# Optimization experiments

Measured on AMD Instinct MI355X. Metric: run time of the kernel, lower is better.

Reference implementation:

```python
import jax, jax.numpy as jnp
import numpy as np


def setup_inputs() -> dict:
    key = jax.random.key(0)
    kq, kk, kv = jax.random.split(key, 3)
    B, S, D = 4, 4096, 128
    q = jax.random.normal(kq, (B, S, D), dtype=jnp.float32)
    k = jax.random.normal(kk, (B, S, D), dtype=jnp.float32)
    v = jax.random.normal(kv, (B, S, D), dtype=jnp.float32)
    return {"q_proj": q, "k_proj": k, "v_proj": v}


def reference(q_proj, k_proj, v_proj):
    # FlashAttention's online-softmax tiling computes exactly standard
    # softmax attention: softmax(Q K^T / sqrt(d)) V (no mask, non-causal).
    d = q_proj.shape[-1]
    scale = 1.0 / jnp.sqrt(jnp.asarray(d, dtype=q_proj.dtype))
    logits = jnp.einsum('bqd,bkd->bqk', q_proj, k_proj) * scale
    probs = jax.nn.softmax(logits, axis=-1)  # numerically stable (max-subtracted)
    out = jnp.einsum('bqk,bkd->bqd', probs, v_proj)
    return out
```

## Files before the change

kernel.cpp:

```cpp
#include <hip/hip_runtime.h>

#define BATCH 4
#define SEQ   4096
#define DIM   128
#define BM    64
#define BN    64
#define NGROUP 2
#define TPG (SEQ / (BN * NGROUP))

#define KS_STRIDE 128
#define VT_STRIDE 72

typedef __attribute__((ext_vector_type(8))) __bf16 bf16x8;
typedef __attribute__((ext_vector_type(8))) unsigned short u16x8;
typedef __attribute__((ext_vector_type(4))) unsigned int u32x4;
typedef __attribute__((ext_vector_type(4))) float f32x4;

__device__ __forceinline__ unsigned short f2bf(float f) {
    __bf16 h = (__bf16)f;
    return __builtin_bit_cast(unsigned short, h);
}

__device__ __forceinline__ bf16x8 lds_frag(const unsigned short* p) {
    u16x8 t = *(const u16x8*)p;
    return __builtin_bit_cast(bf16x8, t);
}

#define LDS_U16 (64 * KS_STRIDE + 128 * VT_STRIDE)

extern "C" __global__ __launch_bounds__(256, 2)
void fa_part(const float* __restrict__ q, const float* __restrict__ k,
             const float* __restrict__ v, float* __restrict__ out,
             float* __restrict__ lsum)
{
    __shared__ __align__(16) unsigned short lds[LDS_U16];
    unsigned short* Ks = lds;
    unsigned short* Vt = lds + 64 * KS_STRIDE;

    const int tid  = threadIdx.x;
    const int wq   = tid >> 6;
    const int lane = tid & 63;
    const int l16  = lane & 15;
    const int quad = lane >> 4;

    const int bid = blockIdx.x;
    const int c   = bid & 7;
    const int b   = c >> 1;
    const int g   = c & 1;
    const int q0  = (bid >> 3) * BM;

    const float scale = 0.08838834764831845f;

    const float4* q4 = (const float4*)q;
    const float4* k4 = (const float4*)k;

    bf16x8 qfrag[4];
#pragma unroll
    for (int kc = 0; kc < 4; ++kc) {
        const float4* qp = &q4[(b * SEQ + q0 + wq * 16 + l16) * 32 + kc * 8 + quad * 2];
        float4 f0 = qp[0], f1 = qp[1];
        u16x8 u;
        u[0] = f2bf(f0.x * scale); u[1] = f2bf(f0.y * scale);
        u[2] = f2bf(f0.z * scale); u[3] = f2bf(f0.w * scale);
        u[4] = f2bf(f1.x * scale); u[5] = f2bf(f1.y * scale);
        u[6] = f2bf(f1.z * scale); u[7] = f2bf(f1.w * scale);
        qfrag[kc] = __builtin_bit_cast(bf16x8, u);
    }

    const int kv0 = g * (SEQ / NGROUP);

    float4 ldK[8];
    float  ldV[4][8];
#pragma unroll
    for (int i = 0; i < 8; ++i) {
        int idx = tid + i * 256;
        ldK[i] = k4[(b * SEQ + kv0 + (idx >> 5)) * 32 + (idx & 31)];
    }
#pragma unroll
    for (int i = 0; i < 4; ++i) {
        int j = tid + i * 256, f = j & 127, kp8 = j >> 7;
        const float* vp = v + (size_t)(b * SEQ + kv0 + kp8 * 8) * DIM + f;
#pragma unroll
        for (int e = 0; e < 8; ++e) ldV[i][e] = vp[e * DIM];
    }

    float l_part = 0.f;
    f32x4 accO[8];
#pragma unroll
    for (int ob = 0; ob < 8; ++ob) accO[ob] = (f32x4){0.f, 0.f, 0.f, 0.f};

    for (int t = 0; t < TPG; ++t) {
        __syncthreads();

#pragma unroll
        for (int i = 0; i < 8; ++i) {
            int idx = tid + i * 256;
            int row = idx >> 5, c4 = idx & 31;
            float4 f = ldK[i];
            ushort4 u;
            u.x = f2bf(f.x); u.y = f2bf(f.y); u.z = f2bf(f.z); u.w = f2bf(f.w);
            *(ushort4*)&Ks[row * KS_STRIDE + ((c4 * 4) ^ (8 * (row & 7)))] = u;
        }
#pragma unroll
        for (int i = 0; i < 4; ++i) {
            int j = tid + i * 256, f = j & 127, kp8 = j >> 7;
            u16x8 u;
#pragma unroll
            for (int e = 0; e < 8; ++e) u[e] = f2bf(ldV[i][e]);
            *(u16x8*)&Vt[f * VT_STRIDE + kp8 * 8] = u;
        }
        __syncthreads();

        if (t + 1 < TPG) {
            const int kbase = kv0 + (t + 1) * BN;
#pragma unroll
            for (int i = 0; i < 8; ++i) {
                int idx = tid + i * 256;
                ldK[i] = k4[(b * SEQ + kbase + (idx >> 5)) * 32 + (idx & 31)];
            }
#pragma unroll
            for (int i = 0; i < 4; ++i) {
                int j = tid + i * 256, f = j & 127, kp8 = j >> 7;
                const float* vp = v + (size_t)(b * SEQ + kbase + kp8 * 8) * DIM + f;
#pragma unroll
                for (int e = 0; e < 8; ++e) ldV[i][e] = vp[e * DIM];
            }
        }

        f32x4 sacc[4];
#pragma unroll
        for (int nb = 0; nb < 4; ++nb) sacc[nb] = (f32x4){0.f, 0.f, 0.f, 0.f};
        __builtin_amdgcn_s_setprio(1);
#pragma unroll
        for (int kc = 0; kc < 4; ++kc) {
#pragma unroll
            for (int nb = 0; nb < 4; ++nb) {
                bf16x8 a = lds_frag(&Ks[(nb * 16 + l16) * KS_STRIDE +
                                        ((kc * 32 + quad * 8) ^ (8 * (l16 & 7)))]);
                sacc[nb] = __builtin_amdgcn_mfma_f32_16x16x32_bf16(a, qfrag[kc], sacc[nb], 0, 0, 0);
            }
        }
        __builtin_amdgcn_s_setprio(0);

        unsigned W[4][2];
#pragma unroll
        for (int nb = 0; nb < 4; ++nb)
#pragma unroll
            for (int s = 0; s < 2; ++s) {
                float e0 = __expf(sacc[nb][2 * s]);
                float e1 = __expf(sacc[nb][2 * s + 1]);
                l_part += e0 + e1;
                W[nb][s] = (unsigned)f2bf(e0) | ((unsigned)f2bf(e1) << 16);
            }

#pragma unroll
        for (int kk = 0; kk < 2; ++kk) {
            u32x4 wv;
#pragma unroll
            for (int w = 0; w < 4; ++w) {
                int src = l16 + 16 * (2 * (quad & 1) + (w >> 1));
                unsigned a0 = (unsigned)__shfl((int)W[kk * 2 + 0][w & 1], src);
                unsigned a1 = (unsigned)__shfl((int)W[kk * 2 + 1][w & 1], src);
                wv[w] = (quad & 2) ? a1 : a0;
            }
            bf16x8 pa = __builtin_bit_cast(bf16x8, wv);
            __builtin_amdgcn_s_setprio(1);
#pragma unroll
            for (int ob = 0; ob < 8; ++ob) {
                bf16x8 bb = lds_frag(&Vt[(ob * 16 + l16) * VT_STRIDE + kk * 32 + quad * 8]);
                accO[ob] = __builtin_amdgcn_mfma_f32_16x16x32_bf16(pa, bb, accO[ob], 0, 0, 0);
            }
            __builtin_amdgcn_s_setprio(0);
        }
    }

    {
        float s = l_part;
        s += __shfl_xor(s, 16);
        s += __shfl_xor(s, 32);
        if (quad == 0) atomicAdd(&lsum[b * SEQ + q0 + wq * 16 + l16], s);
    }
#pragma unroll
    for (int r = 0; r < 4; ++r) {
        const int row = b * SEQ + q0 + wq * 16 + quad * 4 + r;
        float* outp = out + (size_t)row * DIM;
#pragma unroll
        for (int ob = 0; ob < 8; ++ob)
            atomicAdd(&outp[ob * 16 + l16], accO[ob][r]);
    }
}

extern "C" __global__ void fa_norm(float* __restrict__ out, const float* __restrict__ lsum)
{
    int i = blockIdx.x * 256 + threadIdx.x;
    float inv = 1.0f / lsum[i >> 5];
    float4* o4 = (float4*)out;
    float4 vv = o4[i];
    vv.x *= inv; vv.y *= inv; vv.z *= inv; vv.w *= inv;
    o4[i] = vv;
}

extern "C" void kernel_launch(void* const* d_in, const int* in_sizes, int n_in,
                              void* d_out, int out_size, void* d_ws, size_t ws_size,
                              hipStream_t stream) {
    const float* q = (const float*)d_in[0];
    const float* k = (const float*)d_in[1];
    const float* v = (const float*)d_in[2];
    float* out  = (float*)d_out;
    float* lsum = (float*)d_ws;

    hipMemsetAsync(out,  0, (size_t)BATCH * SEQ * DIM * sizeof(float), stream);
    hipMemsetAsync(lsum, 0, (size_t)BATCH * SEQ * sizeof(float), stream);

    dim3 grid(BATCH * (SEQ / BM) * NGROUP);
    dim3 block(256);
    hipLaunchKernelGGL(fa_part, grid, block, 0, stream, q, k, v, out, lsum);

    dim3 ngrid((BATCH * SEQ * DIM / 4) / 256);
    hipLaunchKernelGGL(fa_norm, ngrid, dim3(256), 0, stream, out, lsum);
}
```

Before: 155.9 us.

## Fuse KV-split reduction and normalization into one kernel via in-block LDS combine

Result: slower. 162.8 us (+4.4%).

```diff
diff --git a/kernel.cpp b/kernel.cpp
--- a/kernel.cpp
+++ b/kernel.cpp
@@ -3,13 +3,13 @@
 #define BATCH 4
 #define SEQ   4096
 #define DIM   128
-#define BM    64
-#define BN    64
-#define NGROUP 2
-#define TPG (SEQ / (BN * NGROUP))
+#define BM    32
+#define BN    32
+#define TPG   64
 
 #define KS_STRIDE 128
-#define VT_STRIDE 72
+#define VT_STRIDE 40
+#define GRP_LDS (BN * KS_STRIDE + DIM * VT_STRIDE)
 
 typedef __attribute__((ext_vector_type(8))) __bf16 bf16x8;
 typedef __attribute__((ext_vector_type(8))) unsigned short u16x8;
@@ -26,28 +26,28 @@
     return __builtin_bit_cast(bf16x8, t);
 }
 
-#define LDS_U16 (64 * KS_STRIDE + 128 * VT_STRIDE)
+#define LDS_U16 (2 * GRP_LDS)
 
 extern "C" __global__ __launch_bounds__(256, 2)
-void fa_part(const float* __restrict__ q, const float* __restrict__ k,
-             const float* __restrict__ v, float* __restrict__ out,
-             float* __restrict__ lsum)
+void fa_fused(const float* __restrict__ q, const float* __restrict__ k,
+              const float* __restrict__ v, float* __restrict__ out)
 {
     __shared__ __align__(16) unsigned short lds[LDS_U16];
-    unsigned short* Ks = lds;
-    unsigned short* Vt = lds + 64 * KS_STRIDE;
 
     const int tid  = threadIdx.x;
-    const int wq   = tid >> 6;
+    const int sub  = (tid >> 6) & 1;
+    const int grp  = tid >> 7;
+    const int gt   = tid & 127;
     const int lane = tid & 63;
     const int l16  = lane & 15;
     const int quad = lane >> 4;
 
+    unsigned short* Ks = lds + grp * GRP_LDS;
+    unsigned short* Vt = Ks + BN * KS_STRIDE;
+
     const int bid = blockIdx.x;
-    const int c   = bid & 7;
-    const int b   = c >> 1;
-    const int g   = c & 1;
-    const int q0  = (bid >> 3) * BM;
+    const int b   = bid & 3;
+    const int q0  = (bid >> 2) * BM;
 
     const float scale = 0.08838834764831845f;
 
@@ -57,7 +57,7 @@
     bf16x8 qfrag[4];
 #pragma unroll
     for (int kc = 0; kc < 4; ++kc) {
-        const float4* qp = &q4[(b * SEQ + q0 + wq * 16 + l16) * 32 + kc * 8 + quad * 2];
+        const float4* qp = &q4[(b * SEQ + q0 + sub * 16 + l16) * 32 + kc * 8 + quad * 2];
         float4 f0 = qp[0], f1 = qp[1];
         u16x8 u;
         u[0] = f2bf(f0.x * scale); u[1] = f2bf(f0.y * scale);
@@ -67,18 +67,18 @@
         qfrag[kc] = __builtin_bit_cast(bf16x8, u);
     }
 
-    const int kv0 = g * (SEQ / NGROUP);
+    const int kv0 = grp * (SEQ / 2);
 
     float4 ldK[8];
     float  ldV[4][8];
 #pragma unroll
     for (int i = 0; i < 8; ++i) {
-        int idx = tid + i * 256;
+        int idx = gt + i * 128;
         ldK[i] = k4[(b * SEQ + kv0 + (idx >> 5)) * 32 + (idx & 31)];
     }
 #pragma unroll
     for (int i = 0; i < 4; ++i) {
-        int j = tid + i * 256, f = j & 127, kp8 = j >> 7;
+        int j = gt + i * 128, f = j & 127, kp8 = j >> 7;
         const float* vp = v + (size_t)(b * SEQ + kv0 + kp8 * 8) * DIM + f;
 #pragma unroll
         for (int e = 0; e < 8; ++e) ldV[i][e] = vp[e * DIM];
@@ -94,7 +94,7 @@
 
 #pragma unroll
         for (int i = 0; i < 8; ++i) {
-            int idx = tid + i * 256;
+            int idx = gt + i * 128;
             int row = idx >> 5, c4 = idx & 31;
             float4 f = ldK[i];
             ushort4 u;
@@ -103,7 +103,7 @@
         }
 #pragma unroll
         for (int i = 0; i < 4; ++i) {
-            int j = tid + i * 256, f = j & 127, kp8 = j >> 7;
+            int j = gt + i * 128, f = j & 127, kp8 = j >> 7;
             u16x8 u;
 #pragma unroll
             for (int e = 0; e < 8; ++e) u[e] = f2bf(ldV[i][e]);
@@ -115,26 +115,26 @@
             const int kbase = kv0 + (t + 1) * BN;
 #pragma unroll
             for (int i = 0; i < 8; ++i) {
-                int idx = tid + i * 256;
+                int idx = gt + i * 128;
                 ldK[i] = k4[(b * SEQ + kbase + (idx >> 5)) * 32 + (idx & 31)];
             }
 #pragma unroll
             for (int i = 0; i < 4; ++i) {
-                int j = tid + i * 256, f = j & 127, kp8 = j >> 7;
+                int j = gt + i * 128, f = j & 127, kp8 = j >> 7;
                 const float* vp = v + (size_t)(b * SEQ + kbase + kp8 * 8) * DIM + f;
 #pragma unroll
                 for (int e = 0; e < 8; ++e) ldV[i][e] = vp[e * DIM];
             }
         }
 
-        f32x4 sacc[4];
-#pragma unroll
-        for (int nb = 0; nb < 4; ++nb) sacc[nb] = (f32x4){0.f, 0.f, 0.f, 0.f};
+        f32x4 sacc[2];
+        sacc[0] = (f32x4){0.f, 0.f, 0.f, 0.f};
+        sacc[1] = (f32x4){0.f, 0.f, 0.f, 0.f};
         __builtin_amdgcn_s_setprio(1);
 #pragma unroll
         for (int kc = 0; kc < 4; ++kc) {
 #pragma unroll
-            for (int nb = 0; nb < 4; ++nb) {
+            for (int nb = 0; nb < 2; ++nb) {
                 bf16x8 a = lds_frag(&Ks[(nb * 16 + l16) * KS_STRIDE +
                                         ((kc * 32 + quad * 8) ^ (8 * (l16 & 7)))]);
                 sacc[nb] = __builtin_amdgcn_mfma_f32_16x16x32_bf16(a, qfrag[kc], sacc[nb], 0, 0, 0);
@@ -142,9 +142,9 @@
         }
         __builtin_amdgcn_s_setprio(0);
 
-        unsigned W[4][2];
-#pragma unroll
-        for (int nb = 0; nb < 4; ++nb)
+        unsigned W[2][2];
+#pragma unroll
+        for (int nb = 0; nb < 2; ++nb)
 #pragma unroll
             for (int s = 0; s < 2; ++s) {
                 float e0 = __expf(sacc[nb][2 * s]);
@@ -153,51 +153,52 @@
                 W[nb][s] = (unsigned)f2bf(e0) | ((unsigned)f2bf(e1) << 16);
             }
 
-#pragma unroll
-        for (int kk = 0; kk < 2; ++kk) {
-            u32x4 wv;
-#pragma unroll
-            for (int w = 0; w < 4; ++w) {
-                int src = l16 + 16 * (2 * (quad & 1) + (w >> 1));
-                unsigned a0 = (unsigned)__shfl((int)W[kk * 2 + 0][w & 1], src);
-                unsigned a1 = (unsigned)__shfl((int)W[kk * 2 + 1][w & 1], src);
-                wv[w] = (quad & 2) ? a1 : a0;
-            }
-            bf16x8 pa = __builtin_bit_cast(bf16x8, wv);
-            __builtin_amdgcn_s_setprio(1);
-#pragma unroll
-            for (int ob = 0; ob < 8; ++ob) {
-                bf16x8 bb = lds_frag(&Vt[(ob * 16 + l16) * VT_STRIDE + kk * 32 + quad * 8]);
-                accO[ob] = __builtin_amdgcn_mfma_f32_16x16x32_bf16(pa, bb, accO[ob], 0, 0, 0);
-            }
-            __builtin_amdgcn_s_setprio(0);
-        }
-    }
-
-    {
-        float s = l_part;
-        s += __shfl_xor(s, 16);
-        s += __shfl_xor(s, 32);
-        if (quad == 0) atomicAdd(&lsum[b * SEQ + q0 + wq * 16 + l16], s);
-    }
-#pragma unroll
-    for (int r = 0; r < 4; ++r) {
-        const int row = b * SEQ + q0 + wq * 16 + quad * 4 + r;
-        float* outp = out + (size_t)row * DIM;
+        u32x4 wv;
+#pragma unroll
+        for (int w = 0; w < 4; ++w) {
+            int src = l16 + 16 * (2 * (quad & 1) + (w >> 1));
+            unsigned a0 = (unsigned)__shfl((int)W[0][w & 1], src);
+            unsigned a1 = (unsigned)__shfl((int)W[1][w & 1], src);
+            wv[w] = (quad & 2) ? a1 : a0;
+        }
+        bf16x8 pa = __builtin_bit_cast(bf16x8, wv);
+        __builtin_amdgcn_s_setprio(1);
+#pragma unroll
+        for (int ob = 0; ob < 8; ++ob) {
+            bf16x8 bb = lds_frag(&Vt[(ob * 16 + l16) * VT_STRIDE + quad * 8]);
+            accO[ob] = __builtin_amdgcn_mfma_f32_16x16x32_bf16(pa, bb, accO[ob], 0, 0, 0);
+        }
+        __builtin_amdgcn_s_setprio(0);
+    }
+
+    float s = l_part;
+    s += __shfl_xor(s, 16);
+    s += __shfl_xor(s, 32);
+    __syncthreads();
+    float* mbuf = (float*)lds;
+    float* lbuf = mbuf + 32 * 132;
+    if (grp == 1) {
 #pragma unroll
         for (int ob = 0; ob < 8; ++ob)
-            atomicAdd(&outp[ob * 16 + l16], accO[ob][r]);
-    }
-}
-
-extern "C" __global__ void fa_norm(float* __restrict__ out, const float* __restrict__ lsum)
-{
-    int i = blockIdx.x * 256 + threadIdx.x;
-    float inv = 1.0f / lsum[i >> 5];
-    float4* o4 = (float4*)out;
-    float4 vv = o4[i];
-    vv.x *= inv; vv.y *= inv; vv.z *= inv; vv.w *= inv;
-    o4[i] = vv;
+#pragma unroll
+            for (int r = 0; r < 4; ++r)
+                mbuf[(sub * 16 + quad * 4 + r) * 132 + ob * 16 + l16] = accO[ob][r];
+        if (quad == 0) lbuf[sub * 16 + l16] = s;
+    }
+    __syncthreads();
+    if (grp == 0) {
+        float ltot = s + lbuf[sub * 16 + l16];
+#pragma unroll
+        for (int r = 0; r < 4; ++r) {
+            float inv = 1.0f / __shfl(ltot, quad * 4 + r);
+            const int row = sub * 16 + quad * 4 + r;
+            float* outp = out + (size_t)(b * SEQ + q0 + row) * DIM;
+#pragma unroll
+            for (int ob = 0; ob < 8; ++ob)
+                outp[ob * 16 + l16] =
+                    (accO[ob][r] + mbuf[row * 132 + ob * 16 + l16]) * inv;
+        }
+    }
 }
 
 extern "C" void kernel_launch(void* const* d_in, const int* in_sizes, int n_in,
@@ -206,16 +207,9 @@
     const float* q = (const float*)d_in[0];
     const float* k = (const float*)d_in[1];
     const float* v = (const float*)d_in[2];
-    float* out  = (float*)d_out;
-    float* lsum = (float*)d_ws;
-
-    hipMemsetAsync(out,  0, (size_t)BATCH * SEQ * DIM * sizeof(float), stream);
-    hipMemsetAsync(lsum, 0, (size_t)BATCH * SEQ * sizeof(float), stream);
-
-    dim3 grid(BATCH * (SEQ / BM) * NGROUP);
+    float* out = (float*)d_out;
+
+    dim3 grid(BATCH * (SEQ / BM));
     dim3 block(256);
-    hipLaunchKernelGGL(fa_part, grid, block, 0, stream, q, k, v, out, lsum);
-
-    dim3 ngrid((BATCH * SEQ * DIM / 4) / 256);
-    hipLaunchKernelGGL(fa_norm, ngrid, dim3(256), 0, stream, out, lsum);
-}
+    hipLaunchKernelGGL(fa_fused, grid, block, 0, stream, q, k, v, out);
+}
```

## Compute transposed PV with 16x16x16 MFMA, dropping P shuffles and lsum atomics

Applied to the files above, without the earlier changes.

After: 197.9 us. 26.9% more time.

```diff
diff --git a/kernel.cpp b/kernel.cpp
--- a/kernel.cpp
+++ b/kernel.cpp
@@ -13,8 +13,10 @@
 
 typedef __attribute__((ext_vector_type(8))) __bf16 bf16x8;
 typedef __attribute__((ext_vector_type(8))) unsigned short u16x8;
-typedef __attribute__((ext_vector_type(4))) unsigned int u32x4;
 typedef __attribute__((ext_vector_type(4))) float f32x4;
+typedef __attribute__((ext_vector_type(4))) short i16x4;
+
+#define MFMA_PV(a, b, c) __builtin_amdgcn_mfma_f32_16x16x16bf16_1k(a, b, c, 0, 0, 0)
 
 __device__ __forceinline__ unsigned short f2bf(float f) {
     __bf16 h = (__bf16)f;
@@ -85,9 +87,9 @@
     }
 
     float l_part = 0.f;
-    f32x4 accO[8];
-#pragma unroll
-    for (int ob = 0; ob < 8; ++ob) accO[ob] = (f32x4){0.f, 0.f, 0.f, 0.f};
+    f32x4 accT[8];
+#pragma unroll
+    for (int ob = 0; ob < 8; ++ob) accT[ob] = (f32x4){0.f, 0.f, 0.f, 0.f};
 
     for (int t = 0; t < TPG; ++t) {
         __syncthreads();
@@ -142,58 +144,56 @@
         }
         __builtin_amdgcn_s_setprio(0);
 
-        unsigned W[4][2];
-#pragma unroll
-        for (int nb = 0; nb < 4; ++nb)
-#pragma unroll
-            for (int s = 0; s < 2; ++s) {
-                float e0 = __expf(sacc[nb][2 * s]);
-                float e1 = __expf(sacc[nb][2 * s + 1]);
-                l_part += e0 + e1;
-                W[nb][s] = (unsigned)f2bf(e0) | ((unsigned)f2bf(e1) << 16);
-            }
-
-#pragma unroll
-        for (int kk = 0; kk < 2; ++kk) {
-            u32x4 wv;
-#pragma unroll
-            for (int w = 0; w < 4; ++w) {
-                int src = l16 + 16 * (2 * (quad & 1) + (w >> 1));
-                unsigned a0 = (unsigned)__shfl((int)W[kk * 2 + 0][w & 1], src);
-                unsigned a1 = (unsigned)__shfl((int)W[kk * 2 + 1][w & 1], src);
-                wv[w] = (quad & 2) ? a1 : a0;
-            }
-            bf16x8 pa = __builtin_bit_cast(bf16x8, wv);
-            __builtin_amdgcn_s_setprio(1);
-#pragma unroll
-            for (int ob = 0; ob < 8; ++ob) {
-                bf16x8 bb = lds_frag(&Vt[(ob * 16 + l16) * VT_STRIDE + kk * 32 + quad * 8]);
-                accO[ob] = __builtin_amdgcn_mfma_f32_16x16x32_bf16(pa, bb, accO[ob], 0, 0, 0);
-            }
-            __builtin_amdgcn_s_setprio(0);
-        }
+        i16x4 pb[4];
+#pragma unroll
+        for (int nb = 0; nb < 4; ++nb) {
+            float e0 = __expf(sacc[nb][0]);
+            float e1 = __expf(sacc[nb][1]);
+            float e2 = __expf(sacc[nb][2]);
+            float e3 = __expf(sacc[nb][3]);
+            l_part += (e0 + e1) + (e2 + e3);
+            ushort4 u;
+            u.x = f2bf(e0); u.y = f2bf(e1); u.z = f2bf(e2); u.w = f2bf(e3);
+            pb[nb] = __builtin_bit_cast(i16x4, u);
+        }
+
+        __builtin_amdgcn_s_setprio(1);
+#pragma unroll
+        for (int ob = 0; ob < 8; ++ob) {
+            const unsigned short* vb = &Vt[(ob * 16 + l16) * VT_STRIDE + quad * 4];
+#pragma unroll
+            for (int nb = 0; nb < 4; ++nb) {
+                ushort4 raw = *(const ushort4*)(vb + nb * 16);
+                i16x4 av = __builtin_bit_cast(i16x4, raw);
+                accT[ob] = MFMA_PV(av, pb[nb], accT[ob]);
+            }
+        }
+        __builtin_amdgcn_s_setprio(0);
     }
 
     {
         float s = l_part;
         s += __shfl_xor(s, 16);
         s += __shfl_xor(s, 32);
-        if (quad == 0) atomicAdd(&lsum[b * SEQ + q0 + wq * 16 + l16], s);
-    }
-#pragma unroll
-    for (int r = 0; r < 4; ++r) {
-        const int row = b * SEQ + q0 + wq * 16 + quad * 4 + r;
-        float* outp = out + (size_t)row * DIM;
+        if (quad == 0)
+            lsum[(size_t)(b * SEQ + q0 + wq * 16 + l16) * NGROUP + g] = s;
+    }
+    {
+        float* outp = out + (size_t)(b * SEQ + q0 + wq * 16 + l16) * DIM + quad * 4;
 #pragma unroll
         for (int ob = 0; ob < 8; ++ob)
-            atomicAdd(&outp[ob * 16 + l16], accO[ob][r]);
+#pragma unroll
+            for (int r = 0; r < 4; ++r)
+                atomicAdd(&outp[ob * 16 + r], accT[ob][r]);
     }
 }
 
 extern "C" __global__ void fa_norm(float* __restrict__ out, const float* __restrict__ lsum)
 {
     int i = blockIdx.x * 256 + threadIdx.x;
-    float inv = 1.0f / lsum[i >> 5];
+    int row = i >> 5;
+    float2 L = ((const float2*)lsum)[row];
+    float inv = 1.0f / (L.x + L.y);
     float4* o4 = (float4*)out;
     float4 vv = o4[i];
     vv.x *= inv; vv.y *= inv; vv.z *= inv; vv.w *= inv;
@@ -209,8 +209,7 @@
     float* out  = (float*)d_out;
     float* lsum = (float*)d_ws;
 
-    hipMemsetAsync(out,  0, (size_t)BATCH * SEQ * DIM * sizeof(float), stream);
-    hipMemsetAsync(lsum, 0, (size_t)BATCH * SEQ * sizeof(float), stream);
+    (void)hipMemsetAsync(out, 0, (size_t)BATCH * SEQ * DIM * sizeof(float), stream);
 
     dim3 grid(BATCH * (SEQ / BM) * NGROUP);
     dim3 block(256);
```

## Replace atomic split-K output merge with plain partial stores and swizzle V LDS

Applied to the files above, without the earlier changes.

After: 145.5 us. 6.7% less time.

```diff
diff --git a/kernel.cpp b/kernel.cpp
--- a/kernel.cpp
+++ b/kernel.cpp
@@ -9,7 +9,7 @@
 #define TPG (SEQ / (BN * NGROUP))
 
 #define KS_STRIDE 128
-#define VT_STRIDE 72
+#define VT_STRIDE 64
 
 typedef __attribute__((ext_vector_type(8))) __bf16 bf16x8;
 typedef __attribute__((ext_vector_type(8))) unsigned short u16x8;
@@ -31,7 +31,7 @@
 extern "C" __global__ __launch_bounds__(256, 2)
 void fa_part(const float* __restrict__ q, const float* __restrict__ k,
              const float* __restrict__ v, float* __restrict__ out,
-             float* __restrict__ lsum)
+             float* __restrict__ lsum, float* __restrict__ wsO)
 {
     __shared__ __align__(16) unsigned short lds[LDS_U16];
     unsigned short* Ks = lds;
@@ -107,7 +107,7 @@
             u16x8 u;
 #pragma unroll
             for (int e = 0; e < 8; ++e) u[e] = f2bf(ldV[i][e]);
-            *(u16x8*)&Vt[f * VT_STRIDE + kp8 * 8] = u;
+            *(u16x8*)&Vt[f * VT_STRIDE + ((kp8 * 8) ^ (8 * (f & 7)))] = u;
         }
         __syncthreads();
 
@@ -167,7 +167,8 @@
             __builtin_amdgcn_s_setprio(1);
 #pragma unroll
             for (int ob = 0; ob < 8; ++ob) {
-                bf16x8 bb = lds_frag(&Vt[(ob * 16 + l16) * VT_STRIDE + kk * 32 + quad * 8]);
+                bf16x8 bb = lds_frag(&Vt[(ob * 16 + l16) * VT_STRIDE +
+                                         ((kk * 32 + quad * 8) ^ (8 * (l16 & 7)))]);
                 accO[ob] = __builtin_amdgcn_mfma_f32_16x16x32_bf16(pa, bb, accO[ob], 0, 0, 0);
             }
             __builtin_amdgcn_s_setprio(0);
@@ -178,24 +179,43 @@
         float s = l_part;
         s += __shfl_xor(s, 16);
         s += __shfl_xor(s, 32);
-        if (quad == 0) atomicAdd(&lsum[b * SEQ + q0 + wq * 16 + l16], s);
-    }
-#pragma unroll
-    for (int r = 0; r < 4; ++r) {
-        const int row = b * SEQ + q0 + wq * 16 + quad * 4 + r;
-        float* outp = out + (size_t)row * DIM;
-#pragma unroll
-        for (int ob = 0; ob < 8; ++ob)
-            atomicAdd(&outp[ob * 16 + l16], accO[ob][r]);
-    }
-}
-
-extern "C" __global__ void fa_norm(float* __restrict__ out, const float* __restrict__ lsum)
+        if (quad == 0)
+            lsum[(size_t)(b * SEQ + q0 + wq * 16 + l16) * NGROUP + g] = s;
+    }
+    if (wsO) {
+        float* dst = (g == 0) ? out : wsO;
+#pragma unroll
+        for (int r = 0; r < 4; ++r) {
+            float* outp = dst + (size_t)(b * SEQ + q0 + wq * 16 + quad * 4 + r) * DIM;
+#pragma unroll
+            for (int ob = 0; ob < 8; ++ob)
+                outp[ob * 16 + l16] = accO[ob][r];
+        }
+    } else {
+#pragma unroll
+        for (int r = 0; r < 4; ++r) {
+            float* outp = out + (size_t)(b * SEQ + q0 + wq * 16 + quad * 4 + r) * DIM;
+#pragma unroll
+            for (int ob = 0; ob < 8; ++ob)
+                atomicAdd(&outp[ob * 16 + l16], accO[ob][r]);
+        }
+    }
+}
+
+extern "C" __global__ void fa_norm(float* __restrict__ out,
+                                   const float* __restrict__ lsum,
+                                   const float* __restrict__ wsO)
 {
     int i = blockIdx.x * 256 + threadIdx.x;
-    float inv = 1.0f / lsum[i >> 5];
+    int row = i >> 5;
+    float2 L = ((const float2*)lsum)[row];
+    float inv = 1.0f / (L.x + L.y);
     float4* o4 = (float4*)out;
     float4 vv = o4[i];
+    if (wsO) {
+        float4 pv = ((const float4*)wsO)[i];
+        vv.x += pv.x; vv.y += pv.y; vv.z += pv.z; vv.w += pv.w;
+    }
     vv.x *= inv; vv.y *= inv; vv.z *= inv; vv.w *= inv;
     o4[i] = vv;
 }
@@ -207,15 +227,20 @@
     const float* k = (const float*)d_in[1];
     const float* v = (const float*)d_in[2];
     float* out  = (float*)d_out;
+
+    const size_t lsum_bytes = (size_t)BATCH * SEQ * NGROUP * sizeof(float);
+    const size_t part_bytes = (size_t)BATCH * SEQ * DIM * sizeof(float);
     float* lsum = (float*)d_ws;
-
-    hipMemsetAsync(out,  0, (size_t)BATCH * SEQ * DIM * sizeof(float), stream);
-    hipMemsetAsync(lsum, 0, (size_t)BATCH * SEQ * sizeof(float), stream);
+    float* wsO  = (ws_size >= lsum_bytes + part_bytes)
+                ? (float*)((char*)d_ws + lsum_bytes) : nullptr;
+
+    if (!wsO)
+        (void)hipMemsetAsync(out, 0, part_bytes, stream);
 
     dim3 grid(BATCH * (SEQ / BM) * NGROUP);
     dim3 block(256);
-    hipLaunchKernelGGL(fa_part, grid, block, 0, stream, q, k, v, out, lsum);
+    hipLaunchKernelGGL(fa_part, grid, block, 0, stream, q, k, v, out, lsum, wsO);
 
     dim3 ngrid((BATCH * SEQ * DIM / 4) / 256);
-    hipLaunchKernelGGL(fa_norm, ngrid, dim3(256), 0, stream, out, lsum);
-}
+    hipLaunchKernelGGL(fa_norm, ngrid, dim3(256), 0, stream, out, lsum, wsO);
+}
```
